# Kernel optimization log

Measured on AMD Instinct MI355X. Metric: run time of the kernel, lower is better.

The kernel has to match this reference:

```python
import jax, jax.numpy as jnp
import numpy as np


def setup_inputs() -> dict:
    key = jax.random.key(0)
    k1, k2, k3 = jax.random.split(key, 3)
    B, H, I, O, Dp1 = 4, 2048, 1024, 1024, 4  # degree=3 -> degree+1=4
    x = jax.random.normal(k1, (B, H, I, Dp1), dtype=jnp.float32)
    weight = 0.1 * jax.random.normal(k2, (O, Dp1), dtype=jnp.float32)
    weighted_sum = 0.1 * jax.random.normal(k3, (O, I), dtype=jnp.float32)
    return {"x": x, "weight": weight, "weighted_sum": weighted_sum}


def reference(x, weight, weighted_sum):
    # Original: weights[o,i,d] = weighted_sum[o,i] * weight[o,d];
    #           out[b,h,o] = sum_{i,d} x[b,h,i,d] * weights[o,i,d]
    # Fused 3-operand einsum avoids materializing the (O, I, D+1) intermediate.
    return jnp.einsum('bhid,oi,od->bho', x, weighted_sum, weight)
```

## Files before the change

### kernel.cpp

```cpp
#include <hip/hip_runtime.h>

typedef unsigned short u16;
typedef u16 u16x4 __attribute__((ext_vector_type(4)));
typedef float f32x4 __attribute__((ext_vector_type(4)));
typedef __bf16 bf16x8 __attribute__((ext_vector_type(8)));

#define M_DIM 8192
#define N_DIM 1024
#define K_DIM 4096

__device__ __forceinline__ u16 f2bf(float f) {
  unsigned u = __float_as_uint(f);
  u += 0x7FFFu + ((u >> 16) & 1u);
  return (u16)(u >> 16);
}

__global__ __launch_bounds__(256) void k_cvt(const float* __restrict__ x,
                                             u16* __restrict__ y) {
  long i = ((long)blockIdx.x * 256 + threadIdx.x) * 4;
  f32x4 a = *(const f32x4*)(x + i);
  u16x4 r;
  r[0] = f2bf(a[0]); r[1] = f2bf(a[1]); r[2] = f2bf(a[2]); r[3] = f2bf(a[3]);
  *(u16x4*)(y + i) = r;
}

__global__ __launch_bounds__(256) void k_w2(const float* __restrict__ w,
                                            const float* __restrict__ ws,
                                            u16* __restrict__ w2) {
  int idx = blockIdx.x * 256 + threadIdx.x;
  int o = idx >> 10;
  float s = ws[idx];
  f32x4 wv = *(const f32x4*)(w + o * 4);
  u16x4 r;
  r[0] = f2bf(s * wv[0]); r[1] = f2bf(s * wv[1]);
  r[2] = f2bf(s * wv[2]); r[3] = f2bf(s * wv[3]);
  *(u16x4*)(w2 + (size_t)idx * 4) = r;
}

typedef __attribute__((address_space(1))) const void gvoid_t;
typedef __attribute__((address_space(3))) void lvoid_t;
__device__ __forceinline__ void gll16(const void* g, void* l) {
  __builtin_amdgcn_global_load_lds((gvoid_t*)g, (lvoid_t*)l, 16, 0, 0);
}

__global__ __launch_bounds__(512) void k_gemm(const u16* __restrict__ A,
                                              const u16* __restrict__ Bt,
                                              float* __restrict__ C) {
  __shared__ u16 sA[128 * 64];
  __shared__ u16 sB[128 * 64];

  const int t    = threadIdx.x;
  const int lane = t & 63;
  const int wid  = t >> 6;
  const int m0   = blockIdx.y * 128;
  const int n0   = blockIdx.x * 128;

  const int s0 = t, s1 = t + 512;
  const int r0 = s0 >> 3, c0 = (s0 & 7) ^ (r0 & 7);
  const int r1 = s1 >> 3, c1 = (s1 & 7) ^ (r1 & 7);
  const u16* gA0 = A  + (size_t)(m0 + r0) * K_DIM + c0 * 8;
  const u16* gA1 = A  + (size_t)(m0 + r1) * K_DIM + c1 * 8;
  const u16* gB0 = Bt + (size_t)(n0 + r0) * K_DIM + c0 * 8;
  const u16* gB1 = Bt + (size_t)(n0 + r1) * K_DIM + c1 * 8;
  u16* lA0 = sA + s0 * 8;  u16* lA1 = sA + s1 * 8;
  u16* lB0 = sB + s0 * 8;  u16* lB1 = sB + s1 * 8;

  const int wm = (wid >> 1) * 32;
  const int wn = (wid & 1) * 64;
  const int fr = lane & 15;
  const int lc = lane >> 4;

  f32x4 acc[2][4];
#pragma unroll
  for (int i = 0; i < 2; i++)
#pragma unroll
    for (int j = 0; j < 4; j++) acc[i][j] = (f32x4){0.f, 0.f, 0.f, 0.f};

  for (int k0 = 0; k0 < K_DIM; k0 += 64) {
    gll16(gA0, lA0); gll16(gA1, lA1);
    gll16(gB0, lB0); gll16(gB1, lB1);
    gA0 += 64; gA1 += 64; gB0 += 64; gB1 += 64;
    __syncthreads();

#pragma unroll
    for (int ks = 0; ks < 2; ks++) {
      bf16x8 af[2], bf[4];
#pragma unroll
      for (int mi = 0; mi < 2; mi++) {
        int r  = wm + mi * 16 + fr;
        int pc = (ks * 4 + lc) ^ (r & 7);
        af[mi] = *(const bf16x8*)(sA + r * 64 + pc * 8);
      }
#pragma unroll
      for (int ni = 0; ni < 4; ni++) {
        int r  = wn + ni * 16 + fr;
        int pc = (ks * 4 + lc) ^ (r & 7);
        bf[ni] = *(const bf16x8*)(sB + r * 64 + pc * 8);
      }
#pragma unroll
      for (int mi = 0; mi < 2; mi++)
#pragma unroll
        for (int ni = 0; ni < 4; ni++)
          acc[mi][ni] = __builtin_amdgcn_mfma_f32_16x16x32_bf16(
              af[mi], bf[ni], acc[mi][ni], 0, 0, 0);
    }
    __syncthreads();
  }

  const int cr = (lane >> 4) * 4;
  const int cc = lane & 15;
#pragma unroll
  for (int mi = 0; mi < 2; mi++)
#pragma unroll
    for (int ni = 0; ni < 4; ni++) {
      float* cp = C + (size_t)(m0 + wm + mi * 16 + cr) * N_DIM +
                  (n0 + wn + ni * 16 + cc);
#pragma unroll
      for (int r = 0; r < 4; r++) cp[(size_t)r * N_DIM] = acc[mi][ni][r];
    }
}

extern "C" void kernel_launch(void* const* d_in, const int* in_sizes, int n_in,
                              void* d_out, int out_size, void* d_ws, size_t ws_size,
                              hipStream_t stream) {
  const float* x  = (const float*)d_in[0];
  const float* w  = (const float*)d_in[1];
  const float* ws = (const float*)d_in[2];
  float* out = (float*)d_out;

  u16* xbf = (u16*)d_ws;
  u16* w2  = xbf + (size_t)M_DIM * K_DIM;

  k_cvt<<<32768, 256, 0, stream>>>(x, xbf);
  k_w2<<<4096, 256, 0, stream>>>(w, ws, w2);

  dim3 grid(N_DIM / 128, M_DIM / 128);
  k_gemm<<<grid, 512, 0, stream>>>(xbf, w2, out);
}
```

Measured before the change: 278.9 us.

## Fuse fp32-to-bf16 conversion of x into GEMM A-tile loads with swizzled block order

```diff
diff --git a/kernel.cpp b/kernel.cpp
--- a/kernel.cpp
+++ b/kernel.cpp
@@ -4,6 +4,7 @@
 typedef u16 u16x4 __attribute__((ext_vector_type(4)));
 typedef float f32x4 __attribute__((ext_vector_type(4)));
 typedef __bf16 bf16x8 __attribute__((ext_vector_type(8)));
+typedef __bf16 bf16x4 __attribute__((ext_vector_type(4)));
 
 #define M_DIM 8192
 #define N_DIM 1024
@@ -13,15 +14,6 @@
   unsigned u = __float_as_uint(f);
   u += 0x7FFFu + ((u >> 16) & 1u);
   return (u16)(u >> 16);
-}
-
-__global__ __launch_bounds__(256) void k_cvt(const float* __restrict__ x,
-                                             u16* __restrict__ y) {
-  long i = ((long)blockIdx.x * 256 + threadIdx.x) * 4;
-  f32x4 a = *(const f32x4*)(x + i);
-  u16x4 r;
-  r[0] = f2bf(a[0]); r[1] = f2bf(a[1]); r[2] = f2bf(a[2]); r[3] = f2bf(a[3]);
-  *(u16x4*)(y + i) = r;
 }
 
 __global__ __launch_bounds__(256) void k_w2(const float* __restrict__ w,
@@ -43,7 +35,14 @@
   __builtin_amdgcn_global_load_lds((gvoid_t*)g, (lvoid_t*)l, 16, 0, 0);
 }
 
-__global__ __launch_bounds__(512) void k_gemm(const u16* __restrict__ A,
+__device__ __forceinline__ void cvt_store(u16* dst, f32x4 a) {
+  bf16x4 b;
+  b[0] = (__bf16)a[0]; b[1] = (__bf16)a[1];
+  b[2] = (__bf16)a[2]; b[3] = (__bf16)a[3];
+  *(bf16x4*)dst = b;
+}
+
+__global__ __launch_bounds__(512) void k_gemm(const float* __restrict__ A,
                                               const u16* __restrict__ Bt,
                                               float* __restrict__ C) {
   __shared__ u16 sA[128 * 64];
@@ -52,17 +51,24 @@
   const int t    = threadIdx.x;
   const int lane = t & 63;
   const int wid  = t >> 6;
-  const int m0   = blockIdx.y * 128;
-  const int n0   = blockIdx.x * 128;
+
+  const int L  = blockIdx.x;
+  const int xc = L & 7;
+  const int jj = L >> 3;
+  const int m0 = (xc * 8 + (jj >> 3)) * 128;
+  const int n0 = (jj & 7) * 128;
+
+  const int ar  = t >> 4;
+  const int aq  = t & 15;
+  const int apc = (aq >> 1) ^ (ar & 7);
+  const float* pA = A + (size_t)(m0 + ar) * K_DIM + aq * 4;
+  u16* lA = sA + ar * 64 + apc * 8 + (aq & 1) * 4;
 
   const int s0 = t, s1 = t + 512;
   const int r0 = s0 >> 3, c0 = (s0 & 7) ^ (r0 & 7);
   const int r1 = s1 >> 3, c1 = (s1 & 7) ^ (r1 & 7);
-  const u16* gA0 = A  + (size_t)(m0 + r0) * K_DIM + c0 * 8;
-  const u16* gA1 = A  + (size_t)(m0 + r1) * K_DIM + c1 * 8;
   const u16* gB0 = Bt + (size_t)(n0 + r0) * K_DIM + c0 * 8;
   const u16* gB1 = Bt + (size_t)(n0 + r1) * K_DIM + c1 * 8;
-  u16* lA0 = sA + s0 * 8;  u16* lA1 = sA + s1 * 8;
   u16* lB0 = sB + s0 * 8;  u16* lB1 = sB + s1 * 8;
 
   const int wm = (wid >> 1) * 32;
@@ -76,15 +82,31 @@
 #pragma unroll
     for (int j = 0; j < 4; j++) acc[i][j] = (f32x4){0.f, 0.f, 0.f, 0.f};
 
+  f32x4 pf0 = *(const f32x4*)(pA);
+  f32x4 pf1 = *(const f32x4*)(pA + (size_t)32 * K_DIM);
+  f32x4 pf2 = *(const f32x4*)(pA + (size_t)64 * K_DIM);
+  f32x4 pf3 = *(const f32x4*)(pA + (size_t)96 * K_DIM);
+
   for (int k0 = 0; k0 < K_DIM; k0 += 64) {
-    gll16(gA0, lA0); gll16(gA1, lA1);
+    cvt_store(lA,           pf0);
+    cvt_store(lA + 32 * 64, pf1);
+    cvt_store(lA + 64 * 64, pf2);
+    cvt_store(lA + 96 * 64, pf3);
     gll16(gB0, lB0); gll16(gB1, lB1);
-    gA0 += 64; gA1 += 64; gB0 += 64; gB1 += 64;
+    gB0 += 64; gB1 += 64;
     __syncthreads();
+
+    if (k0 + 64 < K_DIM) {
+      pA += 64;
+      pf0 = *(const f32x4*)(pA);
+      pf1 = *(const f32x4*)(pA + (size_t)32 * K_DIM);
+      pf2 = *(const f32x4*)(pA + (size_t)64 * K_DIM);
+      pf3 = *(const f32x4*)(pA + (size_t)96 * K_DIM);
+    }
 
 #pragma unroll
     for (int ks = 0; ks < 2; ks++) {
-      bf16x8 af[2], bf[4];
+      bf16x8 af[2], bfr[4];
 #pragma unroll
       for (int mi = 0; mi < 2; mi++) {
         int r  = wm + mi * 16 + fr;
@@ -95,14 +117,14 @@
       for (int ni = 0; ni < 4; ni++) {
         int r  = wn + ni * 16 + fr;
         int pc = (ks * 4 + lc) ^ (r & 7);
-        bf[ni] = *(const bf16x8*)(sB + r * 64 + pc * 8);
+        bfr[ni] = *(const bf16x8*)(sB + r * 64 + pc * 8);
       }
 #pragma unroll
       for (int mi = 0; mi < 2; mi++)
 #pragma unroll
         for (int ni = 0; ni < 4; ni++)
           acc[mi][ni] = __builtin_amdgcn_mfma_f32_16x16x32_bf16(
-              af[mi], bf[ni], acc[mi][ni], 0, 0, 0);
+              af[mi], bfr[ni], acc[mi][ni], 0, 0, 0);
     }
     __syncthreads();
   }
@@ -128,12 +150,8 @@
   const float* ws = (const float*)d_in[2];
   float* out = (float*)d_out;
 
-  u16* xbf = (u16*)d_ws;
-  u16* w2  = xbf + (size_t)M_DIM * K_DIM;
+  u16* w2 = (u16*)d_ws;
 
-  k_cvt<<<32768, 256, 0, stream>>>(x, xbf);
   k_w2<<<4096, 256, 0, stream>>>(w, ws, w2);
-
-  dim3 grid(N_DIM / 128, M_DIM / 128);
-  k_gemm<<<grid, 512, 0, stream>>>(xbf, w2, out);
+  k_gemm<<<512, 512, 0, stream>>>(x, w2, out);
 }
```

Result: faster. 271.8 us (-2.5%).

## Fuse fp32-to-bf16 conversion of x into GEMM with register-staged double buffering

Applied to the files above, without the earlier changes.

```diff
diff --git a/kernel.cpp b/kernel.cpp
--- a/kernel.cpp
+++ b/kernel.cpp
@@ -2,26 +2,21 @@
 
 typedef unsigned short u16;
 typedef u16 u16x4 __attribute__((ext_vector_type(4)));
+typedef u16 u16x8 __attribute__((ext_vector_type(8)));
 typedef float f32x4 __attribute__((ext_vector_type(4)));
 typedef __bf16 bf16x8 __attribute__((ext_vector_type(8)));
 
 #define M_DIM 8192
 #define N_DIM 1024
 #define K_DIM 4096
+#define BM 128
+#define BN 256
+#define BK 32
 
 __device__ __forceinline__ u16 f2bf(float f) {
   unsigned u = __float_as_uint(f);
   u += 0x7FFFu + ((u >> 16) & 1u);
   return (u16)(u >> 16);
-}
-
-__global__ __launch_bounds__(256) void k_cvt(const float* __restrict__ x,
-                                             u16* __restrict__ y) {
-  long i = ((long)blockIdx.x * 256 + threadIdx.x) * 4;
-  f32x4 a = *(const f32x4*)(x + i);
-  u16x4 r;
-  r[0] = f2bf(a[0]); r[1] = f2bf(a[1]); r[2] = f2bf(a[2]); r[3] = f2bf(a[3]);
-  *(u16x4*)(y + i) = r;
 }
 
 __global__ __launch_bounds__(256) void k_w2(const float* __restrict__ w,
@@ -37,80 +32,120 @@
   *(u16x4*)(w2 + (size_t)idx * 4) = r;
 }
 
-typedef __attribute__((address_space(1))) const void gvoid_t;
-typedef __attribute__((address_space(3))) void lvoid_t;
-__device__ __forceinline__ void gll16(const void* g, void* l) {
-  __builtin_amdgcn_global_load_lds((gvoid_t*)g, (lvoid_t*)l, 16, 0, 0);
+
+__device__ __forceinline__ void bar() {
+  asm volatile("s_waitcnt lgkmcnt(0)" ::: "memory");
+  __builtin_amdgcn_s_barrier();
 }
 
-__global__ __launch_bounds__(512) void k_gemm(const u16* __restrict__ A,
-                                              const u16* __restrict__ Bt,
-                                              float* __restrict__ C) {
-  __shared__ u16 sA[128 * 64];
-  __shared__ u16 sB[128 * 64];
+__global__ __launch_bounds__(512, 2) void k_gemm(const float* __restrict__ A,
+                                                 const u16* __restrict__ Bt,
+                                                 float* __restrict__ C) {
+  __shared__ u16 sA[2][BM * BK];
+  __shared__ u16 sB[2][BN * BK];
 
   const int t    = threadIdx.x;
   const int lane = t & 63;
   const int wid  = t >> 6;
-  const int m0   = blockIdx.y * 128;
-  const int n0   = blockIdx.x * 128;
 
-  const int s0 = t, s1 = t + 512;
-  const int r0 = s0 >> 3, c0 = (s0 & 7) ^ (r0 & 7);
-  const int r1 = s1 >> 3, c1 = (s1 & 7) ^ (r1 & 7);
-  const u16* gA0 = A  + (size_t)(m0 + r0) * K_DIM + c0 * 8;
-  const u16* gA1 = A  + (size_t)(m0 + r1) * K_DIM + c1 * 8;
-  const u16* gB0 = Bt + (size_t)(n0 + r0) * K_DIM + c0 * 8;
-  const u16* gB1 = Bt + (size_t)(n0 + r1) * K_DIM + c1 * 8;
-  u16* lA0 = sA + s0 * 8;  u16* lA1 = sA + s1 * 8;
-  u16* lB0 = sB + s0 * 8;  u16* lB1 = sB + s1 * 8;
+  const int L   = blockIdx.x;
+  const int xcd = L & 7;
+  const int jb  = L >> 3;
+  const int m0  = (xcd * 8 + (jb >> 2)) * BM;
+  const int n0  = (jb & 3) * BN;
 
-  const int wm = (wid >> 1) * 32;
-  const int wn = (wid & 1) * 64;
-  const int fr = lane & 15;
-  const int lc = lane >> 4;
+  const int ra = t >> 2, qa = t & 3;
+  const float* gA = A + (size_t)(m0 + ra) * K_DIM + qa * 8;
+  const int wAoff = ra * 32 + (qa ^ ((ra >> 1) & 3)) * 8;
 
-  f32x4 acc[2][4];
+  const int rb = t >> 1, ub = t & 1;
+  const u16* gB = Bt + (size_t)(n0 + rb) * K_DIM + ub * 16;
+  const int mbs = (rb >> 1) & 3;
+  const int wB0off = rb * 32 + ((2 * ub) ^ mbs) * 8;
+  const int wB1off = rb * 32 + ((2 * ub + 1) ^ mbs) * 8;
+
+  const int wm  = (wid >> 2) * 64;
+  const int wn  = (wid & 3) * 64;
+  const int fr  = lane & 15;
+  const int lc  = lane >> 4;
+  const int fsl = (lc ^ ((fr >> 1) & 3)) * 8;
+
+  f32x4 acc[4][4];
 #pragma unroll
-  for (int i = 0; i < 2; i++)
+  for (int i = 0; i < 4; i++)
 #pragma unroll
     for (int j = 0; j < 4; j++) acc[i][j] = (f32x4){0.f, 0.f, 0.f, 0.f};
 
-  for (int k0 = 0; k0 < K_DIM; k0 += 64) {
-    gll16(gA0, lA0); gll16(gA1, lA1);
-    gll16(gB0, lB0); gll16(gB1, lB1);
-    gA0 += 64; gA1 += 64; gB0 += 64; gB1 += 64;
-    __syncthreads();
+  f32x4 a0_0, a0_1, a1_0, a1_1;
+  u16x8 b0_0, b0_1, b1_0, b1_1;
 
-#pragma unroll
-    for (int ks = 0; ks < 2; ks++) {
-      bf16x8 af[2], bf[4];
-#pragma unroll
-      for (int mi = 0; mi < 2; mi++) {
-        int r  = wm + mi * 16 + fr;
-        int pc = (ks * 4 + lc) ^ (r & 7);
-        af[mi] = *(const bf16x8*)(sA + r * 64 + pc * 8);
-      }
-#pragma unroll
-      for (int ni = 0; ni < 4; ni++) {
-        int r  = wn + ni * 16 + fr;
-        int pc = (ks * 4 + lc) ^ (r & 7);
-        bf[ni] = *(const bf16x8*)(sB + r * 64 + pc * 8);
-      }
-#pragma unroll
-      for (int mi = 0; mi < 2; mi++)
-#pragma unroll
-        for (int ni = 0; ni < 4; ni++)
-          acc[mi][ni] = __builtin_amdgcn_mfma_f32_16x16x32_bf16(
-              af[mi], bf[ni], acc[mi][ni], 0, 0, 0);
-    }
-    __syncthreads();
+#define ISSUE(aX0, aX1, bX0, bX1)       \
+  do {                                  \
+    aX0 = *(const f32x4*)(gA);          \
+    aX1 = *(const f32x4*)(gA + 4);      \
+    bX0 = *(const u16x8*)(gB);          \
+    bX1 = *(const u16x8*)(gB + 8);      \
+    gA += BK; gB += BK;                 \
+  } while (0)
+
+#define WRITE(buf, aX0, aX1, bX0, bX1)               \
+  do {                                               \
+    bf16x8 av;                                       \
+    av[0] = (__bf16)aX0[0]; av[1] = (__bf16)aX0[1];  \
+    av[2] = (__bf16)aX0[2]; av[3] = (__bf16)aX0[3];  \
+    av[4] = (__bf16)aX1[0]; av[5] = (__bf16)aX1[1];  \
+    av[6] = (__bf16)aX1[2]; av[7] = (__bf16)aX1[3];  \
+    *(bf16x8*)(sA[buf] + wAoff) = av;                \
+    *(u16x8*)(sB[buf] + wB0off) = bX0;               \
+    *(u16x8*)(sB[buf] + wB1off) = bX1;               \
+  } while (0)
+
+#define COMPUTE(buf)                                                     \
+  do {                                                                   \
+    bf16x8 af[4], bfv[4];                                                \
+    _Pragma("unroll")                                                    \
+    for (int mi = 0; mi < 4; mi++)                                       \
+      af[mi] = *(const bf16x8*)(sA[buf] + (wm + mi * 16 + fr) * 32 + fsl); \
+    _Pragma("unroll")                                                    \
+    for (int ni = 0; ni < 4; ni++)                                       \
+      bfv[ni] = *(const bf16x8*)(sB[buf] + (wn + ni * 16 + fr) * 32 + fsl); \
+    _Pragma("unroll")                                                    \
+    for (int mi = 0; mi < 4; mi++)                                       \
+      _Pragma("unroll")                                                  \
+      for (int ni = 0; ni < 4; ni++)                                     \
+        acc[mi][ni] = __builtin_amdgcn_mfma_f32_16x16x32_bf16(           \
+            af[mi], bfv[ni], acc[mi][ni], 0, 0, 0);                      \
+  } while (0)
+
+  ISSUE(a0_0, a0_1, b0_0, b0_1);
+  ISSUE(a1_0, a1_1, b1_0, b1_1);
+  WRITE(0, a0_0, a0_1, b0_0, b0_1);
+  bar();
+
+  for (int jj = 0; jj < 63; ++jj) {
+    ISSUE(a0_0, a0_1, b0_0, b0_1);
+    COMPUTE(0);
+    WRITE(1, a1_0, a1_1, b1_0, b1_1);
+    bar();
+    ISSUE(a1_0, a1_1, b1_0, b1_1);
+    COMPUTE(1);
+    WRITE(0, a0_0, a0_1, b0_0, b0_1);
+    bar();
   }
+
+  COMPUTE(0);
+  WRITE(1, a1_0, a1_1, b1_0, b1_1);
+  bar();
+  COMPUTE(1);
+
+#undef ISSUE
+#undef WRITE
+#undef COMPUTE
 
   const int cr = (lane >> 4) * 4;
   const int cc = lane & 15;
 #pragma unroll
-  for (int mi = 0; mi < 2; mi++)
+  for (int mi = 0; mi < 4; mi++)
 #pragma unroll
     for (int ni = 0; ni < 4; ni++) {
       float* cp = C + (size_t)(m0 + wm + mi * 16 + cr) * N_DIM +
@@ -128,12 +163,8 @@
   const float* ws = (const float*)d_in[2];
   float* out = (float*)d_out;
 
-  u16* xbf = (u16*)d_ws;
-  u16* w2  = xbf + (size_t)M_DIM * K_DIM;
+  u16* w2 = (u16*)d_ws;
 
-  k_cvt<<<32768, 256, 0, stream>>>(x, xbf);
   k_w2<<<4096, 256, 0, stream>>>(w, ws, w2);
-
-  dim3 grid(N_DIM / 128, M_DIM / 128);
-  k_gemm<<<grid, 512, 0, stream>>>(xbf, w2, out);
+  k_gemm<<<256, 512, 0, stream>>>(x, w2, out);
 }
```

Result: no change. 284.1 us (+1.8%).

## Pipeline GEMM with triple-buffered LDS, 256x128 tiles and XCD-aware block mapping

Applied to the files above, without the earlier changes.

```diff
diff --git a/kernel.cpp b/kernel.cpp
--- a/kernel.cpp
+++ b/kernel.cpp
@@ -8,6 +8,9 @@
 #define M_DIM 8192
 #define N_DIM 1024
 #define K_DIM 4096
+#define BM 256
+#define BN 128
+#define BK 32
 
 __device__ __forceinline__ u16 f2bf(float f) {
   unsigned u = __float_as_uint(f);
@@ -43,74 +46,116 @@
   __builtin_amdgcn_global_load_lds((gvoid_t*)g, (lvoid_t*)l, 16, 0, 0);
 }
 
-__global__ __launch_bounds__(512) void k_gemm(const u16* __restrict__ A,
-                                              const u16* __restrict__ Bt,
-                                              float* __restrict__ C) {
-  __shared__ u16 sA[128 * 64];
-  __shared__ u16 sB[128 * 64];
+__global__ __launch_bounds__(512, 4) void k_gemm(const u16* __restrict__ A,
+                                                 const u16* __restrict__ Bt,
+                                                 float* __restrict__ C) {
+  __shared__ u16 lds[32768];
+  u16* const sA0 = lds;
+  u16* const sA1 = lds + 8192;
+  u16* const sA2 = lds + 16384;
+  u16* const sB0 = lds + 24576;
+  u16* const sB1 = lds + 28672;
 
   const int t    = threadIdx.x;
   const int lane = t & 63;
   const int wid  = t >> 6;
-  const int m0   = blockIdx.y * 128;
-  const int n0   = blockIdx.x * 128;
 
-  const int s0 = t, s1 = t + 512;
-  const int r0 = s0 >> 3, c0 = (s0 & 7) ^ (r0 & 7);
-  const int r1 = s1 >> 3, c1 = (s1 & 7) ^ (r1 & 7);
-  const u16* gA0 = A  + (size_t)(m0 + r0) * K_DIM + c0 * 8;
-  const u16* gA1 = A  + (size_t)(m0 + r1) * K_DIM + c1 * 8;
-  const u16* gB0 = Bt + (size_t)(n0 + r0) * K_DIM + c0 * 8;
-  const u16* gB1 = Bt + (size_t)(n0 + r1) * K_DIM + c1 * 8;
-  u16* lA0 = sA + s0 * 8;  u16* lA1 = sA + s1 * 8;
-  u16* lB0 = sB + s0 * 8;  u16* lB1 = sB + s1 * 8;
+  const int L   = blockIdx.x;
+  const int xcd = L & 7;
+  const int jb  = L >> 3;
+  const int m0  = (xcd * 4 + (jb >> 3)) * BM;
+  const int n0  = (jb & 7) * BN;
 
-  const int wm = (wid >> 1) * 32;
+  const u16* gA0; const u16* gA1; int dA0, dA1;
+  {
+    int s = t,       r = s >> 2, cg = (s & 3) ^ (r & 3);
+    gA0 = A + (size_t)(m0 + r) * K_DIM + cg * 8;  dA0 = s * 8;
+    s = 512 + t;     r = s >> 2; cg = (s & 3) ^ (r & 3);
+    gA1 = A + (size_t)(m0 + r) * K_DIM + cg * 8;  dA1 = s * 8;
+  }
+  const u16* gB; int dBo;
+  {
+    int s = t, r = s >> 2, cg = (s & 3) ^ (r & 3);
+    gB = Bt + (size_t)(n0 + r) * K_DIM + cg * 8;  dBo = s * 8;
+  }
+
+  const int wm = (wid >> 1) * 64;
   const int wn = (wid & 1) * 64;
   const int fr = lane & 15;
   const int lc = lane >> 4;
 
-  f32x4 acc[2][4];
+  f32x4 acc[4][4];
 #pragma unroll
-  for (int i = 0; i < 2; i++)
+  for (int i = 0; i < 4; i++)
 #pragma unroll
     for (int j = 0; j < 4; j++) acc[i][j] = (f32x4){0.f, 0.f, 0.f, 0.f};
 
-  for (int k0 = 0; k0 < K_DIM; k0 += 64) {
-    gll16(gA0, lA0); gll16(gA1, lA1);
-    gll16(gB0, lB0); gll16(gB1, lB1);
-    gA0 += 64; gA1 += 64; gB0 += 64; gB1 += 64;
-    __syncthreads();
+  gll16(gA0, sA0 + dA0); gll16(gA1, sA0 + dA1);
+  gll16(gB,  sB0 + dBo);
+  gll16(gA0 + 32, sA1 + dA0); gll16(gA1 + 32, sA1 + dA1);
+  asm volatile("s_waitcnt vmcnt(2)" ::: "memory");
+  __builtin_amdgcn_s_barrier();
 
+  u16 *pAc = sA0, *pAn = sA1, *pAs = sA2;
+  u16 *pBc = sB0, *pBs = sB1;
+
+#define AREAD(dst, MI)                                                     \
+  do {                                                                     \
+    int r_ = wm + (MI) * 16 + fr;                                          \
+    dst = *(const bf16x8*)(pAc + r_ * 32 + ((lc ^ (r_ & 3)) * 8));         \
+  } while (0)
+
+  for (int tt = 0; tt < 128; ++tt) {
+    const int ka = ((tt + 2) & 127) * BK;
+    const int kb = ((tt + 1) & 127) * BK;
+    bf16x8 af0, af1, bq[4];
+
+    AREAD(af0, 0); AREAD(af1, 1);
 #pragma unroll
-    for (int ks = 0; ks < 2; ks++) {
-      bf16x8 af[2], bf[4];
+    for (int n_ = 0; n_ < 4; n_++) {
+      int r_ = wn + n_ * 16 + fr;
+      bq[n_] = *(const bf16x8*)(pBc + r_ * 32 + ((lc ^ (r_ & 3)) * 8));
+    }
+    gll16(gB + kb, pBs + dBo);
+    __builtin_amdgcn_s_barrier();
+    asm volatile("s_waitcnt lgkmcnt(0)" ::: "memory");
+    __builtin_amdgcn_s_setprio(1);
 #pragma unroll
-      for (int mi = 0; mi < 2; mi++) {
-        int r  = wm + mi * 16 + fr;
-        int pc = (ks * 4 + lc) ^ (r & 7);
-        af[mi] = *(const bf16x8*)(sA + r * 64 + pc * 8);
-      }
+    for (int n_ = 0; n_ < 4; n_++) {
+      acc[0][n_] = __builtin_amdgcn_mfma_f32_16x16x32_bf16(af0, bq[n_],
+                                                           acc[0][n_], 0, 0, 0);
+      acc[1][n_] = __builtin_amdgcn_mfma_f32_16x16x32_bf16(af1, bq[n_],
+                                                           acc[1][n_], 0, 0, 0);
+    }
+    __builtin_amdgcn_s_setprio(0);
+    __builtin_amdgcn_s_barrier();
+
+    AREAD(af0, 2); AREAD(af1, 3);
+    gll16(gA0 + ka, pAs + dA0); gll16(gA1 + ka, pAs + dA1);
+    asm volatile("s_waitcnt vmcnt(2)" ::: "memory");
+    __builtin_amdgcn_s_barrier();
+    asm volatile("s_waitcnt lgkmcnt(0)" ::: "memory");
+    __builtin_amdgcn_s_setprio(1);
 #pragma unroll
-      for (int ni = 0; ni < 4; ni++) {
-        int r  = wn + ni * 16 + fr;
-        int pc = (ks * 4 + lc) ^ (r & 7);
-        bf[ni] = *(const bf16x8*)(sB + r * 64 + pc * 8);
-      }
-#pragma unroll
-      for (int mi = 0; mi < 2; mi++)
-#pragma unroll
-        for (int ni = 0; ni < 4; ni++)
-          acc[mi][ni] = __builtin_amdgcn_mfma_f32_16x16x32_bf16(
-              af[mi], bf[ni], acc[mi][ni], 0, 0, 0);
+    for (int n_ = 0; n_ < 4; n_++) {
+      acc[2][n_] = __builtin_amdgcn_mfma_f32_16x16x32_bf16(af0, bq[n_],
+                                                           acc[2][n_], 0, 0, 0);
+      acc[3][n_] = __builtin_amdgcn_mfma_f32_16x16x32_bf16(af1, bq[n_],
+                                                           acc[3][n_], 0, 0, 0);
     }
-    __syncthreads();
+    __builtin_amdgcn_s_setprio(0);
+    __builtin_amdgcn_s_barrier();
+
+    u16* tmp = pAc; pAc = pAn; pAn = pAs; pAs = tmp;
+    tmp = pBc; pBc = pBs; pBs = tmp;
   }
+
+#undef AREAD
 
   const int cr = (lane >> 4) * 4;
   const int cc = lane & 15;
 #pragma unroll
-  for (int mi = 0; mi < 2; mi++)
+  for (int mi = 0; mi < 4; mi++)
 #pragma unroll
     for (int ni = 0; ni < 4; ni++) {
       float* cp = C + (size_t)(m0 + wm + mi * 16 + cr) * N_DIM +
@@ -133,7 +178,5 @@
 
   k_cvt<<<32768, 256, 0, stream>>>(x, xbf);
   k_w2<<<4096, 256, 0, stream>>>(w, ws, w2);
-
-  dim3 grid(N_DIM / 128, M_DIM / 128);
-  k_gemm<<<grid, 512, 0, stream>>>(xbf, w2, out);
+  k_gemm<<<256, 512, 0, stream>>>(xbf, w2, out);
 }
```

After: 281.7 us. Within noise of the previous version (+1.0%).
